# Optimization experiments

Measured on AMD Instinct MI355X. Metric: run time of the kernel, lower is better.

The kernel has to match this reference:

```python
import jax, jax.numpy as jnp
import numpy as np

E = 8          # num_experts
K = 2          # top-k experts per token
CAP_RATIO = 1.05


def setup_inputs() -> dict:
    key = jax.random.key(0)
    k0, k1, k2, k3 = jax.random.split(key, 4)
    B, S, D, H = 2, 2048, 512, 2048
    return {
        "x": jax.random.normal(k0, (B, S, D), jnp.float32),
        "gate_w": jax.random.normal(k1, (E, D), jnp.float32) * (1.0 / np.sqrt(D)),
        "fc1_w": jax.random.normal(k2, (E, D, H), jnp.float32) * (1.0 / np.sqrt(D)),
        "fc1_b": jnp.zeros((E, H), jnp.float32),
        "fc2_w": jax.random.normal(k3, (E, H, D), jnp.float32) * (1.0 / np.sqrt(H)),
        "fc2_b": jnp.zeros((E, D), jnp.float32),
    }


def reference(x, gate_w, fc1_w, fc1_b, fc2_w, fc2_b):
    B, S, D = x.shape
    xf = x.reshape(-1, D)               # [T, D]
    T = xf.shape[0]

    # ---- router (eval mode: no noise) ----
    logits = xf @ gate_w.T              # [T, E]
    gates = jax.nn.softmax(logits, axis=-1)
    top_g, top_i = jax.lax.top_k(gates, K)   # [T, K]

    # importance auxiliary loss (std unbiased=False == jnp.std default)
    imp = gates.sum(axis=0)                  # [E]
    imp_loss = (jnp.std(imp) / (imp.mean() + 1e-6)) ** 2

    # ---- capacity-limited dispatch mask ----
    # torch loops slot-major: slot 0 over all tokens in order, then slot 1.
    # position of each (slot, token) entry within its expert's queue:
    buffer_cap = round(K * T * CAP_RATIO / E)
    idx_sm = top_i.T.reshape(-1)                        # [K*T] slot-major
    oh = jax.nn.one_hot(idx_sm, E, dtype=jnp.int32)     # [K*T, E]
    pos = jnp.cumsum(oh, axis=0) - oh                   # earlier same-expert count
    pos_e = jnp.take_along_axis(pos, idx_sm[:, None], axis=1)[:, 0]
    within = (pos_e < buffer_cap).reshape(K, T).T       # [T, K] bool

    wf = within.astype(xf.dtype)
    oh_tke = jax.nn.one_hot(top_i, E, dtype=xf.dtype) * wf[..., None]  # dispatch mask [T,K,E]
    combine_te = jnp.einsum('tk,tke->te', top_g * wf, oh_tke / jnp.maximum(oh_tke, 1e-30) * oh_tke) if False else jnp.einsum('tk,tke->te', top_g * wf, jax.nn.one_hot(top_i, E, dtype=xf.dtype))

    # load-balance loss from post-capacity token counts
    tokens_per_expert = oh_tke.sum(axis=(0, 1))         # [E]
    l_load = (jnp.std(tokens_per_expert) / (tokens_per_expert.mean() + 1e-6)) ** 2
    l_aux = 0.5 * (imp_loss + l_load)

    # ---- per-expert MLP (dense compute, masked combine) ----
    h = jnp.einsum('td,edh->teh', xf, fc1_w) + fc1_b[None]      # [T, E, H]
    h = jax.nn.gelu(h, approximate=False)                       # torch nn.GELU default
    y = jnp.einsum('teh,ehd->ted', h, fc2_w) + fc2_b[None]      # [T, E, D]

    out = jnp.einsum('te,ted->td', combine_te, y).reshape(B, S, D)
    return out, l_aux, l_load
```

## Files before the change

### kernel.cpp

```cpp
#include <hip/hip_runtime.h>
#include <hip/hip_bf16.h>

#define E_    8
#define TT    4096
#define DD    512
#define HH    2048
#define CAP   1075
#define MPAD  1152
#define MT    9
#define MT2   18

typedef __bf16 bf16_t;
typedef bf16_t bf16x4 __attribute__((ext_vector_type(4)));
typedef bf16_t bf16x8 __attribute__((ext_vector_type(8)));
typedef float  f32x4  __attribute__((ext_vector_type(4)));
typedef unsigned int u32;

__device__ __forceinline__ bf16_t tobf(float f) { return (bf16_t)f; }

__device__ __forceinline__ float gelu_f(float v) {
  const float u = v * (0.7978845608028654f + 0.035677408136300125f * v * v);
  const float a = __builtin_fabsf(u);
  const float ex = __expf(2.0f * a);
  float th = 1.0f - 2.0f / (ex + 1.0f);
  th = __builtin_copysignf(th, u);
  return 0.5f * v * (1.0f + th);
}

#define OFF_ETOK  256u
#define OFF_TOPI  (OFF_ETOK + 8u*1152u*4u)
#define OFF_TOPG  (OFF_TOPI + 4096u*2u*4u)
#define OFF_SLOT  (OFF_TOPG + 4096u*2u*4u)
#define OFF_XB    (OFF_SLOT + 4096u*2u*4u)
#define XB_BYTES  (4096u*512u*2u)
#define OFF_W1T   (OFF_XB + XB_BYTES)
#define W1T_BYTES (8u*512u*2048u*2u)
#define OFF_W2T   (OFF_W1T + W1T_BYTES)
#define W2T_BYTES (8u*2048u*512u*2u)
#define OFF_H     (OFF_W2T + W2T_BYTES)
#define H_BYTES   (8u*1152u*2048u*2u)
#define OFF_Y     OFF_W1T

__global__ __launch_bounds__(256) void router_kernel(
    const float* __restrict__ x, const float* __restrict__ gw,
    float* __restrict__ imp, int* __restrict__ top_i, float* __restrict__ top_g,
    bf16_t* __restrict__ xb) {
  const int tid = threadIdx.x;
  const int wid = tid >> 6, lane = tid & 63;
  const int t = blockIdx.x * 4 + wid;

  float p[E_];
#pragma unroll
  for (int e = 0; e < E_; ++e) p[e] = 0.f;
  const float* xr = x + (size_t)t * DD;
  bf16_t* xo = xb + (size_t)t * DD;
#pragma unroll
  for (int it = 0; it < 2; ++it) {
    const int d = it * 256 + lane * 4;
    const float4 xv = *(const float4*)(xr + d);
    bf16_t o4[4] = {tobf(xv.x), tobf(xv.y), tobf(xv.z), tobf(xv.w)};
    *(bf16x4*)(xo + d) = *(const bf16x4*)o4;
#pragma unroll
    for (int e = 0; e < E_; ++e) {
      const float4 gv = *(const float4*)(gw + e * DD + d);
      p[e] += xv.x * gv.x + xv.y * gv.y + xv.z * gv.z + xv.w * gv.w;
    }
  }
#pragma unroll
  for (int off = 32; off > 0; off >>= 1) {
#pragma unroll
    for (int e = 0; e < E_; ++e) p[e] += __shfl_down(p[e], off);
  }

  __shared__ float simp[4][E_];
  if (lane == 0) {
    float mx = p[0];
#pragma unroll
    for (int e = 1; e < E_; ++e) mx = fmaxf(mx, p[e]);
    float g[E_]; float s = 0.f;
#pragma unroll
    for (int e = 0; e < E_; ++e) { g[e] = expf(p[e] - mx); s += g[e]; }
    const float inv = 1.f / s;
#pragma unroll
    for (int e = 0; e < E_; ++e) { g[e] *= inv; simp[wid][e] = g[e]; }
    int i0 = 0;
#pragma unroll
    for (int e = 1; e < E_; ++e) if (g[e] > g[i0]) i0 = e;
    int i1 = (i0 == 0) ? 1 : 0;
#pragma unroll
    for (int e = 0; e < E_; ++e) if (e != i0 && g[e] > g[i1]) i1 = e;
    top_i[t * 2 + 0] = i0;  top_i[t * 2 + 1] = i1;
    top_g[t * 2 + 0] = g[i0]; top_g[t * 2 + 1] = g[i1];
  }
  __syncthreads();
  if (tid < E_) {
    const float s = simp[0][tid] + simp[1][tid] + simp[2][tid] + simp[3][tid];
    atomicAdd(&imp[tid], s);
  }
}

__global__ __launch_bounds__(1024) void capacity_kernel(
    const int* __restrict__ top_i, const float* __restrict__ top_g,
    const float* __restrict__ imp, int* __restrict__ etok,
    int* __restrict__ slot_map, int* __restrict__ kept, float* __restrict__ scal) {
  __shared__ u32 wt[16][4];
  const int tid = threadIdx.x, wave = tid >> 6, lane = tid & 63;

  int eidx[8];
#pragma unroll
  for (int q = 0; q < 8; ++q) {
    const int j = tid * 8 + q;
    const int k = j >> 12, t = j & (TT - 1);
    eidx[q] = top_i[t * 2 + k];
  }
  u32 pk[4] = {0u, 0u, 0u, 0u};
#pragma unroll
  for (int q = 0; q < 8; ++q) pk[eidx[q] >> 1] += 1u << ((eidx[q] & 1) * 16);

  u32 v[4] = {pk[0], pk[1], pk[2], pk[3]};
#pragma unroll
  for (int off = 1; off < 64; off <<= 1) {
#pragma unroll
    for (int p = 0; p < 4; ++p) {
      const u32 n = (u32)__shfl_up((int)v[p], off);
      if (lane >= off) v[p] += n;
    }
  }
  if (lane == 63) {
#pragma unroll
    for (int p = 0; p < 4; ++p) wt[wave][p] = v[p];
  }
  __syncthreads();
  u32 base[4] = {0u, 0u, 0u, 0u}, tot[4] = {0u, 0u, 0u, 0u};
#pragma unroll
  for (int w = 0; w < 16; ++w) {
#pragma unroll
    for (int p = 0; p < 4; ++p) {
      const u32 xv = wt[w][p];
      if (w < wave) base[p] += xv;
      tot[p] += xv;
    }
  }
  int run[E_];
#pragma unroll
  for (int p = 0; p < 4; ++p) {
    const u32 excl = base[p] + v[p] - pk[p];
    run[2 * p]     = (int)(excl & 0xFFFFu);
    run[2 * p + 1] = (int)(excl >> 16);
  }
#pragma unroll
  for (int q = 0; q < 8; ++q) {
    const int e = eidx[q];
    const int pos = run[e]++;
    const int j = tid * 8 + q;
    if (pos < CAP) {
      const int k = j >> 12, t = j & (TT - 1);
      etok[e * MPAD + pos] = t;
      slot_map[j] = (e << 16) | pos;
    } else {
      slot_map[j] = -1;
    }
  }
  if (tid == 0) {
    float tpe[E_];
#pragma unroll
    for (int p = 0; p < 4; ++p) {
      const int t0 = (int)(tot[p] & 0xFFFFu), t1 = (int)(tot[p] >> 16);
      const int k0 = t0 < CAP ? t0 : CAP, k1 = t1 < CAP ? t1 : CAP;
      kept[2 * p] = k0; kept[2 * p + 1] = k1;
      tpe[2 * p] = (float)k0; tpe[2 * p + 1] = (float)k1;
    }
    float ms = 0.f;
#pragma unroll
    for (int e = 0; e < E_; ++e) ms += tpe[e];
    ms *= (1.f / E_);
    float vt = 0.f;
#pragma unroll
    for (int e = 0; e < E_; ++e) { const float d = tpe[e] - ms; vt += d * d; }
    vt *= (1.f / E_);
    const float ll = vt / ((ms + 1e-6f) * (ms + 1e-6f));

    float iv[E_], mi = 0.f;
#pragma unroll
    for (int e = 0; e < E_; ++e) { iv[e] = imp[e]; mi += iv[e]; }
    mi *= (1.f / E_);
    float vi = 0.f;
#pragma unroll
    for (int e = 0; e < E_; ++e) { const float d = iv[e] - mi; vi += d * d; }
    vi *= (1.f / E_);
    const float il = vi / ((mi + 1e-6f) * (mi + 1e-6f));

    scal[0] = 0.5f * (il + ll);
    scal[1] = ll;
  }
}

__global__ __launch_bounds__(256) void transpose_both_kernel(
    const float* __restrict__ fc1, bf16_t* __restrict__ w1t,
    const float* __restrict__ fc2, bf16_t* __restrict__ w2t) {
  __shared__ float tile[64][65];
  const int z = blockIdx.z;
  const bool first = (z < 8);
  const int e = first ? z : z - 8;
  const int R = first ? DD : HH;
  const int C = first ? HH : DD;
  const int ct = first ? blockIdx.x : blockIdx.y;
  const int rt = first ? blockIdx.y : blockIdx.x;
  const float* ip = (first ? fc1 : fc2) + (size_t)e * DD * HH;
  bf16_t* op = (first ? w1t : w2t) + (size_t)e * DD * HH;
  const int r0 = rt * 64, c0 = ct * 64;
  const int tid = threadIdx.x;
  const int rr = tid >> 4, c4 = (tid & 15) * 4;
#pragma unroll
  for (int p = 0; p < 4; ++p) {
    const int r = p * 16 + rr;
    const float4 v = *(const float4*)(ip + (size_t)(r0 + r) * C + c0 + c4);
    tile[r][c4 + 0] = v.x; tile[r][c4 + 1] = v.y;
    tile[r][c4 + 2] = v.z; tile[r][c4 + 3] = v.w;
  }
  __syncthreads();
  const int g = tid & 7, ob = tid >> 3;
#pragma unroll
  for (int p = 0; p < 2; ++p) {
    const int oc = p * 32 + ob;
    bf16_t o8[8];
#pragma unroll
    for (int k = 0; k < 8; ++k) o8[k] = tobf(tile[g * 8 + k][oc]);
    *(bf16x8*)(op + (size_t)(c0 + oc) * R + r0 + g * 8) = *(const bf16x8*)o8;
  }
}

template <int NW, int MR, int NC, int MI, int KSUB, int KLEN, int KSTR, bool GATHER>
__device__ __forceinline__ void gemm_core(
    const bf16_t* __restrict__ Abase, const int* __restrict__ rows,
    const bf16_t* __restrict__ B,
    bf16_t* As, bf16_t* Bs, f32x4 (&acc)[4][MI]) {
  constexpr int NWC = NC / 64;
  constexpr int AIW = MR / (8 * NW);
  constexpr int BIW = NC / (8 * NW);
  const int tid = threadIdx.x;
  const int wave = tid >> 6, lane = tid & 63;
  const int r8 = lane >> 3;
  const int kswz = ((lane & 7) ^ r8) * 8;
  const bf16_t* ga[AIW];
#pragma unroll
  for (int p = 0; p < AIW; ++p) {
    const int r = (wave * AIW + p) * 8 + r8;
    const int trow = GATHER ? rows[r] : r;
    ga[p] = Abase + (size_t)trow * KSTR + kswz;
  }
  const bf16_t* gb = B + (size_t)(wave * BIW * 8 + r8) * KSTR + kswz;
  const int mw = (wave / NWC) * (MI * 16), nw = (wave % NWC) * 64;
  const int l15 = lane & 15, quad = lane >> 4;
  const int sw = l15 & 7;

  for (int kb = 0; kb < KLEN; kb += KSUB * 64) {
    __syncthreads();
#pragma unroll
    for (int ks = 0; ks < KSUB; ++ks) {
      const int k0 = kb + ks * 64;
#pragma unroll
      for (int p = 0; p < AIW; ++p)
        __builtin_amdgcn_global_load_lds(
            (const __attribute__((address_space(1))) void*)(ga[p] + k0),
            (__attribute__((address_space(3))) void*)(As + (ks * MR + (wave * AIW + p) * 8) * 64),
            16, 0, 0);
#pragma unroll
      for (int p = 0; p < BIW; ++p)
        __builtin_amdgcn_global_load_lds(
            (const __attribute__((address_space(1))) void*)(gb + (size_t)p * 8 * KSTR + k0),
            (__attribute__((address_space(3))) void*)(Bs + (ks * NC + (wave * BIW + p) * 8) * 64),
            16, 0, 0);
    }
    __syncthreads();
#pragma unroll
    for (int kh = 0; kh < KSUB * 2; ++kh) {
      const int kt = kh >> 1;
      const int kc = (((kh & 1) * 4 + quad) ^ sw) << 3;
      bf16x8 af[MI], bfr[4];
#pragma unroll
      for (int i = 0; i < MI; ++i)
        af[i] = *(const bf16x8*)(As + (kt * MR + mw + i * 16 + l15) * 64 + kc);
#pragma unroll
      for (int j = 0; j < 4; ++j)
        bfr[j] = *(const bf16x8*)(Bs + (kt * NC + nw + j * 16 + l15) * 64 + kc);
#pragma unroll
      for (int j = 0; j < 4; ++j)
#pragma unroll
        for (int i = 0; i < MI; ++i)
          acc[j][i] = __builtin_amdgcn_mfma_f32_16x16x32_bf16(bfr[j], af[i], acc[j][i], 0, 0, 0);
    }
  }
}

__global__ __launch_bounds__(512, 4) void gemm1_kernel(
    const bf16_t* __restrict__ xb, const int* __restrict__ etok,
    const int* __restrict__ kept, const bf16_t* __restrict__ W1t,
    const float* __restrict__ b1, bf16_t* __restrict__ Hbuf) {
  const int e = blockIdx.x, tileN = blockIdx.y, tileM = blockIdx.z;
  if (tileM * 128 >= kept[e]) return;
  __shared__ __align__(16) bf16_t As[128 * 64];
  __shared__ __align__(16) bf16_t Bs[256 * 64];
  const bf16_t* B = W1t + ((size_t)e * HH + tileN * 256) * DD;
  f32x4 acc[4][4];
  const f32x4 z = {0.f, 0.f, 0.f, 0.f};
#pragma unroll
  for (int j = 0; j < 4; ++j)
#pragma unroll
    for (int i = 0; i < 4; ++i) acc[j][i] = z;
  gemm_core<8, 128, 256, 4, 1, DD, DD, true>(xb, etok + e * MPAD + tileM * 128, B, As, Bs, acc);

  const int tid = threadIdx.x, wave = tid >> 6, lane = tid & 63;
  const int mw = (wave >> 2) * 64, nw = (wave & 3) * 64;
  const int l15 = lane & 15, quad = lane >> 4;
#pragma unroll
  for (int j = 0; j < 4; ++j) {
    const int n0 = tileN * 256 + nw + j * 16 + quad * 4;
    const float4 b4 = *(const float4*)(b1 + e * HH + n0);
#pragma unroll
    for (int i = 0; i < 4; ++i) {
      const int m = tileM * 128 + mw + i * 16 + l15;
      bf16x4 h4;
      h4.x = tobf(gelu_f(acc[j][i][0] + b4.x));
      h4.y = tobf(gelu_f(acc[j][i][1] + b4.y));
      h4.z = tobf(gelu_f(acc[j][i][2] + b4.z));
      h4.w = tobf(gelu_f(acc[j][i][3] + b4.w));
      *(bf16x4*)(Hbuf + ((size_t)e * MPAD + m) * HH + n0) = h4;
    }
  }
}

__global__ __launch_bounds__(256, 4) void gemm2_kernel(
    const bf16_t* __restrict__ Hbuf, const bf16_t* __restrict__ W2t,
    const int* __restrict__ kept, bf16_t* __restrict__ Ybuf) {
  const int e = blockIdx.x, tileN = blockIdx.y, tileM = blockIdx.z;
  const int nk = kept[e];
  if (tileM * 64 >= nk) return;
  __shared__ __align__(16) bf16_t As[2 * 64 * 64];
  __shared__ __align__(16) bf16_t Bs[2 * 128 * 64];
  const bf16_t* A = Hbuf + ((size_t)e * MPAD + tileM * 64) * HH;
  const bf16_t* B = W2t + ((size_t)e * DD + tileN * 128) * HH;
  f32x4 acc[4][2];
  const f32x4 z = {0.f, 0.f, 0.f, 0.f};
#pragma unroll
  for (int j = 0; j < 4; ++j)
#pragma unroll
    for (int i = 0; i < 2; ++i) acc[j][i] = z;
  gemm_core<4, 64, 128, 2, 2, HH, HH, false>(A, nullptr, B, As, Bs, acc);

  const int tid = threadIdx.x, wave = tid >> 6, lane = tid & 63;
  const int mw = (wave >> 1) * 32, nw = (wave & 1) * 64;
  const int l15 = lane & 15, quad = lane >> 4;
#pragma unroll
  for (int j = 0; j < 4; ++j) {
    const int n0 = tileN * 128 + nw + j * 16 + quad * 4;
#pragma unroll
    for (int i = 0; i < 2; ++i) {
      const int m = tileM * 64 + mw + i * 16 + l15;
      if (m < nk) {
        bf16x4 o4;
        o4.x = tobf(acc[j][i][0]);
        o4.y = tobf(acc[j][i][1]);
        o4.z = tobf(acc[j][i][2]);
        o4.w = tobf(acc[j][i][3]);
        *(bf16x4*)(Ybuf + ((size_t)e * MPAD + m) * DD + n0) = o4;
      }
    }
  }
}

__global__ __launch_bounds__(128) void combine_kernel(
    const bf16_t* __restrict__ Ybuf, const float* __restrict__ b2,
    const int* __restrict__ slot_map, const float* __restrict__ top_g,
    float* __restrict__ out) {
  const int t = blockIdx.x;
  const int c = threadIdx.x * 4;
  float4 acc = {0.f, 0.f, 0.f, 0.f};
#pragma unroll
  for (int k = 0; k < 2; ++k) {
    const int sm = slot_map[k * TT + t];
    if (sm >= 0) {
      const int e = sm >> 16, pos = sm & 0xFFFF;
      const float w = top_g[t * 2 + k];
      const bf16x4 y4 = *(const bf16x4*)(Ybuf + ((size_t)e * MPAD + pos) * DD + c);
      const float4 bb = *(const float4*)(b2 + e * DD + c);
      acc.x += w * ((float)y4.x + bb.x);
      acc.y += w * ((float)y4.y + bb.y);
      acc.z += w * ((float)y4.z + bb.z);
      acc.w += w * ((float)y4.w + bb.w);
    }
  }
  *(float4*)(out + (size_t)t * DD + c) = acc;
}

extern "C" void kernel_launch(void* const* d_in, const int* in_sizes, int n_in,
                              void* d_out, int out_size, void* d_ws, size_t ws_size,
                              hipStream_t stream) {
  const float* x      = (const float*)d_in[0];
  const float* gate_w = (const float*)d_in[1];
  const float* fc1_w  = (const float*)d_in[2];
  const float* fc1_b  = (const float*)d_in[3];
  const float* fc2_w  = (const float*)d_in[4];
  const float* fc2_b  = (const float*)d_in[5];
  float* out = (float*)d_out;

  char* ws = (char*)d_ws;
  float*  imp   = (float*)(ws + 0);
  int*    kept  = (int*)(ws + 64);
  int*    etok  = (int*)(ws + OFF_ETOK);
  int*    top_i = (int*)(ws + OFF_TOPI);
  float*  top_g = (float*)(ws + OFF_TOPG);
  int*    slotm = (int*)(ws + OFF_SLOT);
  bf16_t* xb    = (bf16_t*)(ws + OFF_XB);
  bf16_t* W1t   = (bf16_t*)(ws + OFF_W1T);
  bf16_t* W2t   = (bf16_t*)(ws + OFF_W2T);
  bf16_t* Hbuf  = (bf16_t*)(ws + OFF_H);
  bf16_t* Ybuf  = (bf16_t*)(ws + OFF_Y);
  float*  scal  = out + (size_t)TT * DD;

  hipMemsetAsync(ws, 0, OFF_TOPI, stream);

  transpose_both_kernel<<<dim3(32, 8, 16), 256, 0, stream>>>(fc1_w, W1t, fc2_w, W2t);

  router_kernel<<<TT / 4, 256, 0, stream>>>(x, gate_w, imp, top_i, top_g, xb);
  capacity_kernel<<<1, 1024, 0, stream>>>(top_i, top_g, imp, etok, slotm, kept, scal);

  gemm1_kernel<<<dim3(E_, HH / 256, MT), 512, 0, stream>>>(xb, etok, kept, W1t, fc1_b, Hbuf);
  gemm2_kernel<<<dim3(E_, DD / 128, MT2), 256, 0, stream>>>(Hbuf, W2t, kept, Ybuf);
  combine_kernel<<<TT, 128, 0, stream>>>(Ybuf, fc2_b, slotm, top_g, out);
}
```

Baseline: 219.8 us.

## Double-buffer GEMM LDS loads with vmcnt waits and shrink gemm1 N tile

Replaces the load-then-compute loop in the shared GEMM core with a two-stage ping-pong pipeline. Each K-step's global-to-LDS loads are issued ahead and waited on with explicit s_waitcnt vmcnt and raw barriers, so memory latency overlaps MFMA work. gemm1's N tile is halved to 128 to fit two buffers in LDS, which doubles its grid and re-reads the A tile more often. The hand-written waitcnt counts assume a fixed number of outstanding loads per stage and can break if the compiler emits other vector-memory ops.

```diff
diff --git a/kernel.cpp b/kernel.cpp
--- a/kernel.cpp
+++ b/kernel.cpp
@@ -25,6 +25,18 @@
   float th = 1.0f - 2.0f / (ex + 1.0f);
   th = __builtin_copysignf(th, u);
   return 0.5f * v * (1.0f + th);
+}
+
+template <int N> __device__ __forceinline__ void waitcnt_vm() {
+  static_assert(N == 0 || N == 4 || N == 6, "unsupported vmcnt");
+  if constexpr (N == 0) asm volatile("s_waitcnt vmcnt(0)" ::: "memory");
+  else if constexpr (N == 4) asm volatile("s_waitcnt vmcnt(4)" ::: "memory");
+  else if constexpr (N == 6) asm volatile("s_waitcnt vmcnt(6)" ::: "memory");
+}
+__device__ __forceinline__ void block_barrier() {
+  asm volatile("" ::: "memory");
+  __builtin_amdgcn_s_barrier();
+  asm volatile("" ::: "memory");
 }
 
 #define OFF_ETOK  256u
@@ -230,7 +242,7 @@
   }
 }
 
-template <int NW, int MR, int NC, int MI, int KSUB, int KLEN, int KSTR, bool GATHER>
+template <int NW, int MR, int NC, int MI, int KLEN, int KSTR, bool GATHER>
 __device__ __forceinline__ void gemm_core(
     const bf16_t* __restrict__ Abase, const int* __restrict__ rows,
     const bf16_t* __restrict__ B,
@@ -238,6 +250,11 @@
   constexpr int NWC = NC / 64;
   constexpr int AIW = MR / (8 * NW);
   constexpr int BIW = NC / (8 * NW);
+  constexpr int L   = AIW + BIW;
+  constexpr int NS  = KLEN / 64;
+  constexpr int ABUF = MR * 64;
+  constexpr int BBUF = NC * 64;
+  static_assert(NS >= 2, "need >=2 K-steps");
   const int tid = threadIdx.x;
   const int wave = tid >> 6, lane = tid & 63;
   const int r8 = lane >> 3;
@@ -254,41 +271,60 @@
   const int l15 = lane & 15, quad = lane >> 4;
   const int sw = l15 & 7;
 
-  for (int kb = 0; kb < KLEN; kb += KSUB * 64) {
-    __syncthreads();
-#pragma unroll
-    for (int ks = 0; ks < KSUB; ++ks) {
-      const int k0 = kb + ks * 64;
-#pragma unroll
-      for (int p = 0; p < AIW; ++p)
-        __builtin_amdgcn_global_load_lds(
-            (const __attribute__((address_space(1))) void*)(ga[p] + k0),
-            (__attribute__((address_space(3))) void*)(As + (ks * MR + (wave * AIW + p) * 8) * 64),
-            16, 0, 0);
-#pragma unroll
-      for (int p = 0; p < BIW; ++p)
-        __builtin_amdgcn_global_load_lds(
-            (const __attribute__((address_space(1))) void*)(gb + (size_t)p * 8 * KSTR + k0),
-            (__attribute__((address_space(3))) void*)(Bs + (ks * NC + (wave * BIW + p) * 8) * 64),
-            16, 0, 0);
-    }
-    __syncthreads();
-#pragma unroll
-    for (int kh = 0; kh < KSUB * 2; ++kh) {
-      const int kt = kh >> 1;
-      const int kc = (((kh & 1) * 4 + quad) ^ sw) << 3;
+  auto stage = [&](int s) {
+    const int k0 = s * 64;
+    bf16_t* as = As + (s & 1) * ABUF;
+    bf16_t* bs = Bs + (s & 1) * BBUF;
+#pragma unroll
+    for (int p = 0; p < AIW; ++p)
+      __builtin_amdgcn_global_load_lds(
+          (const __attribute__((address_space(1))) void*)(ga[p] + k0),
+          (__attribute__((address_space(3))) void*)(as + ((wave * AIW + p) * 8) * 64),
+          16, 0, 0);
+#pragma unroll
+    for (int p = 0; p < BIW; ++p)
+      __builtin_amdgcn_global_load_lds(
+          (const __attribute__((address_space(1))) void*)(gb + (size_t)p * 8 * KSTR + k0),
+          (__attribute__((address_space(3))) void*)(bs + ((wave * BIW + p) * 8) * 64),
+          16, 0, 0);
+  };
+  auto compute = [&](int s) {
+    const bf16_t* as = As + (s & 1) * ABUF;
+    const bf16_t* bs = Bs + (s & 1) * BBUF;
+#pragma unroll
+    for (int kh = 0; kh < 2; ++kh) {
+      const int kc = ((kh * 4 + quad) ^ sw) << 3;
       bf16x8 af[MI], bfr[4];
 #pragma unroll
       for (int i = 0; i < MI; ++i)
-        af[i] = *(const bf16x8*)(As + (kt * MR + mw + i * 16 + l15) * 64 + kc);
+        af[i] = *(const bf16x8*)(as + (mw + i * 16 + l15) * 64 + kc);
 #pragma unroll
       for (int j = 0; j < 4; ++j)
-        bfr[j] = *(const bf16x8*)(Bs + (kt * NC + nw + j * 16 + l15) * 64 + kc);
+        bfr[j] = *(const bf16x8*)(bs + (nw + j * 16 + l15) * 64 + kc);
 #pragma unroll
       for (int j = 0; j < 4; ++j)
 #pragma unroll
         for (int i = 0; i < MI; ++i)
           acc[j][i] = __builtin_amdgcn_mfma_f32_16x16x32_bf16(bfr[j], af[i], acc[j][i], 0, 0, 0);
+    }
+  };
+
+  stage(0);
+  stage(1);
+  waitcnt_vm<L>();
+  block_barrier();
+
+#pragma unroll
+  for (int s = 0; s < NS; ++s) {
+    compute(s);
+    block_barrier();
+    if (s + 2 < NS) {
+      stage(s + 2);
+      waitcnt_vm<L>();
+      block_barrier();
+    } else if (s + 1 < NS) {
+      waitcnt_vm<0>();
+      block_barrier();
     }
   }
 }
@@ -299,26 +335,26 @@
     const float* __restrict__ b1, bf16_t* __restrict__ Hbuf) {
   const int e = blockIdx.x, tileN = blockIdx.y, tileM = blockIdx.z;
   if (tileM * 128 >= kept[e]) return;
-  __shared__ __align__(16) bf16_t As[128 * 64];
-  __shared__ __align__(16) bf16_t Bs[256 * 64];
-  const bf16_t* B = W1t + ((size_t)e * HH + tileN * 256) * DD;
-  f32x4 acc[4][4];
+  __shared__ __align__(16) bf16_t As[2 * 128 * 64];
+  __shared__ __align__(16) bf16_t Bs[2 * 128 * 64];
+  const bf16_t* B = W1t + ((size_t)e * HH + tileN * 128) * DD;
+  f32x4 acc[4][2];
   const f32x4 z = {0.f, 0.f, 0.f, 0.f};
 #pragma unroll
   for (int j = 0; j < 4; ++j)
 #pragma unroll
-    for (int i = 0; i < 4; ++i) acc[j][i] = z;
-  gemm_core<8, 128, 256, 4, 1, DD, DD, true>(xb, etok + e * MPAD + tileM * 128, B, As, Bs, acc);
+    for (int i = 0; i < 2; ++i) acc[j][i] = z;
+  gemm_core<8, 128, 128, 2, DD, DD, true>(xb, etok + e * MPAD + tileM * 128, B, As, Bs, acc);
 
   const int tid = threadIdx.x, wave = tid >> 6, lane = tid & 63;
-  const int mw = (wave >> 2) * 64, nw = (wave & 3) * 64;
+  const int mw = (wave >> 1) * 32, nw = (wave & 1) * 64;
   const int l15 = lane & 15, quad = lane >> 4;
 #pragma unroll
   for (int j = 0; j < 4; ++j) {
-    const int n0 = tileN * 256 + nw + j * 16 + quad * 4;
+    const int n0 = tileN * 128 + nw + j * 16 + quad * 4;
     const float4 b4 = *(const float4*)(b1 + e * HH + n0);
 #pragma unroll
-    for (int i = 0; i < 4; ++i) {
+    for (int i = 0; i < 2; ++i) {
       const int m = tileM * 128 + mw + i * 16 + l15;
       bf16x4 h4;
       h4.x = tobf(gelu_f(acc[j][i][0] + b4.x));
@@ -346,7 +382,7 @@
   for (int j = 0; j < 4; ++j)
 #pragma unroll
     for (int i = 0; i < 2; ++i) acc[j][i] = z;
-  gemm_core<4, 64, 128, 2, 2, HH, HH, false>(A, nullptr, B, As, Bs, acc);
+  gemm_core<4, 64, 128, 2, HH, HH, false>(A, nullptr, B, As, Bs, acc);
 
   const int tid = threadIdx.x, wave = tid >> 6, lane = tid & 63;
   const int mw = (wave >> 1) * 32, nw = (wave & 1) * 64;
@@ -425,7 +461,7 @@
   router_kernel<<<TT / 4, 256, 0, stream>>>(x, gate_w, imp, top_i, top_g, xb);
   capacity_kernel<<<1, 1024, 0, stream>>>(top_i, top_g, imp, etok, slotm, kept, scal);
 
-  gemm1_kernel<<<dim3(E_, HH / 256, MT), 512, 0, stream>>>(xb, etok, kept, W1t, fc1_b, Hbuf);
+  gemm1_kernel<<<dim3(E_, HH / 128, MT), 512, 0, stream>>>(xb, etok, kept, W1t, fc1_b, Hbuf);
   gemm2_kernel<<<dim3(E_, DD / 128, MT2), 256, 0, stream>>>(Hbuf, W2t, kept, Ybuf);
   combine_kernel<<<TT, 128, 0, stream>>>(Ybuf, fc2_b, slotm, top_g, out);
 }
```

Measured after the change: 212.5 us. -3.3%, faster.
